# Optimization experiments

Measured on AMD Instinct MI355X. Metric: run time of the kernel, lower is better.

Reference implementation:

```python
import jax, jax.numpy as jnp
import numpy as np
from jax import lax

V = 128     # vocab_size
E = 512     # embed_size
H = 1024    # hidden_size
NE = 10     # num_experts
B = 32
S = 1024


def setup_inputs() -> dict:
    key = jax.random.key(0)
    ks = jax.random.split(key, 11)
    s = 0.05
    return {
        "x": jax.random.randint(ks[0], (B, S), 0, V),
        "emb": jax.random.normal(ks[1], (V, E), jnp.float32) * s,
        "W_ih": jax.random.normal(ks[2], (4 * H, E), jnp.float32) * s,   # gates i,f,g,o
        "W_hh": jax.random.normal(ks[3], (4 * H, H), jnp.float32) * s,
        "b_ih": jax.random.normal(ks[4], (4 * H,), jnp.float32) * s,
        "b_hh": jax.random.normal(ks[5], (4 * H,), jnp.float32) * s,
        "We": jax.random.normal(ks[6], (NE, V, H), jnp.float32) * s,    # expert Linear weights
        "be": jax.random.normal(ks[7], (NE, V), jnp.float32) * s,
        "Wg": jax.random.normal(ks[8], (NE, H), jnp.float32) * s,       # gating Linear
        "bg": jax.random.normal(ks[9], (NE,), jnp.float32) * s,
    }


def _lstm(xe, W_ih, W_hh, b_ih, b_hh):
    # xe: [B,S,E] -> hidden states [B,S,H]; PyTorch LSTM gate order i,f,g,o
    pre = jnp.einsum("bse,ge->bsg", xe, W_ih) + b_ih  # [B,S,4H], input proj hoisted out of scan
    h0 = jnp.zeros((xe.shape[0], H), xe.dtype)
    c0 = jnp.zeros((xe.shape[0], H), xe.dtype)

    def step(carry, p):
        h, c = carry
        g = p + h @ W_hh.T + b_hh
        i, f, gg, o = jnp.split(g, 4, axis=-1)
        c = jax.nn.sigmoid(f) * c + jax.nn.sigmoid(i) * jnp.tanh(gg)
        h = jax.nn.sigmoid(o) * jnp.tanh(c)
        return (h, c), h

    _, hs = lax.scan(step, (h0, c0), pre.transpose(1, 0, 2))  # scan over S
    return hs.transpose(1, 0, 2)  # [B,S,H]


def reference(x, emb, W_ih, W_hh, b_ih, b_hh, We, be, Wg, bg):
    xe = emb[x]                                   # [B,S,E]
    h = _lstm(xe, W_ih, W_hh, b_ih, b_hh)         # [B,S,H]
    # all experts as one batched GEMM: [NE,B,S,V]
    expert_outputs = jnp.einsum("bsh,evh->ebsv", h, We) + be[:, None, None, :]
    gating_weights = jax.nn.softmax(h[:, -1, :] @ Wg.T + bg, axis=-1)  # [B,NE]
    combined = jnp.einsum("be,ebsv->bsv", gating_weights, expert_outputs)
    return combined, expert_outputs, gating_weights
```

## Files before the change

kernel.cpp:

```cpp
#include <hip/hip_runtime.h>
#include <hip/hip_bf16.h>
#include <math.h>

#define V_  128
#define E_  512
#define H_  1024
#define NE_ 10
#define B_  32
#define S_  1024
#define G4H (4*H_)

typedef short bf16x8 __attribute__((ext_vector_type(8)));
typedef float f32x4  __attribute__((ext_vector_type(4)));
typedef int   i32x4  __attribute__((ext_vector_type(4)));

__device__ __forceinline__ short f2bf(float f) {
    __hip_bfloat16 h = __float2bfloat16(f);
    short s; __builtin_memcpy(&s, &h, 2); return s;
}
__device__ __forceinline__ float bf2f(ushort u) {
    unsigned int x = ((unsigned int)u) << 16;
    float f; __builtin_memcpy(&f, &x, 4); return f;
}
__device__ __forceinline__ float sigf(float x) { return 1.f / (1.f + __expf(-x)); }
__device__ __forceinline__ float tanhfast(float x) { return 1.f - 2.f / (__expf(2.f * x) + 1.f); }

__device__ __forceinline__ i32x4 gload4_sc(const void* p) {
    i32x4 r;
    asm volatile("global_load_dwordx4 %0, %1, off sc1" : "=&v"(r) : "v"(p));
    return r;
}
__device__ __forceinline__ void gstore4_sc(void* p, i32x4 v) {
    asm volatile("global_store_dwordx4 %0, %1, off sc1" :: "v"(p), "v"(v) : "memory");
}
__device__ __forceinline__ void gstore1_sc(void* p, int v) {
    asm volatile("global_store_dword %0, %1, off sc1" :: "v"(p), "v"(v) : "memory");
}
#define WAITCNT0() do { asm volatile("s_waitcnt vmcnt(0)" ::: "memory"); \
                        __builtin_amdgcn_sched_barrier(0); } while (0)

__global__ __launch_bounds__(256) void build_T(
    const float* __restrict__ emb, const float* __restrict__ W_ih,
    const float* __restrict__ b_ih, float* __restrict__ T2)
{
    int idx = blockIdx.x * 256 + threadIdx.x;
    int g = idx >> 7, v = idx & 127;
    const float* er = emb + v * E_;
    const float* wr = W_ih + (size_t)g * E_;
    float acc = b_ih[g];
    #pragma unroll 4
    for (int e = 0; e < E_; ++e) acc += er[e] * wr[e];
    T2[v * G4H + (g & 1023) * 4 + (g >> 10)] = acc;
}

__global__ __launch_bounds__(256) void conv_bf16(
    const float* __restrict__ src, ushort* __restrict__ dst, int n)
{
    int i = blockIdx.x * 256 + threadIdx.x;
    if (i < n) dst[i] = (ushort)f2bf(src[i]);
}

__global__ __launch_bounds__(512) void lstm_scan(
    const int* __restrict__ x, const float* __restrict__ T2,
    const float* __restrict__ W_hh, const float* __restrict__ b_hh,
    ushort* __restrict__ hbuf, ushort* __restrict__ h_all, int* __restrict__ flags)
{
    const int p = blockIdx.x;
    const int tid = threadIdx.x;
    const int lane = tid & 63, wave = tid >> 6;
    const int m = lane & 15, kg = lane >> 4;
    const int bh = wave & 1, kq = wave >> 1;

    __shared__ __align__(16) ushort Wl[32 * 1024];
    __shared__ float  part[8 * 512];
    __shared__ __align__(16) float pre_s[32][36];
    __shared__ __align__(16) ushort hstage[256];
    __shared__ float  bhh_l[32];

    #pragma unroll
    for (int i = 0; i < 8; ++i) {
        int grp = tid + i * 512;
        int r = grp >> 7, k8 = (grp & 127) * 8;
        const float* wsrc = W_hh + (size_t)((r & 3) * H_ + p * 8 + (r >> 2)) * H_ + k8;
        float4 w0 = *(const float4*)wsrc;
        float4 w1 = *(const float4*)(wsrc + 4);
        bf16x8 a;
        a[0]=f2bf(w0.x); a[1]=f2bf(w0.y); a[2]=f2bf(w0.z); a[3]=f2bf(w0.w);
        a[4]=f2bf(w1.x); a[5]=f2bf(w1.y); a[6]=f2bf(w1.z); a[7]=f2bf(w1.w);
        *(bf16x8*)&Wl[r * 1024 + (k8 ^ ((r & 7) << 3))] = a;
    }
    if (tid < 32) bhh_l[tid] = b_hh[(tid & 3) * H_ + p * 8 + (tid >> 2)];

    int boff[8];
    #pragma unroll
    for (int kk = 0; kk < 8; ++kk)
        boff[kk] = (bh * 16 + m) * 1024 + kq * 256 + kk * 32 + kg * 8;

    const int eb = tid >> 3, eu = tid & 7;
    float cst = 0.f;
    ushort* hb0 = hbuf;
    ushort* hb1 = hbuf + B_ * H_;
    const int swz = (m & 7) << 3;
    __syncthreads();

    for (int t = 0; t < S_; ++t) {
        const ushort* hrd = (t & 1) ? hb0 : hb1;
        ushort*       hwr = (t & 1) ? hb1 : hb0;

        {
            const int src = kq * 32 + (lane & 31);
            const int* fp = flags + src * 16;
            for (;;) {
                int f;
                asm volatile("global_load_dword %0, %1, off sc1\n\ts_waitcnt vmcnt(0)"
                             : "=&v"(f) : "v"(fp) : "memory");
                __builtin_amdgcn_sched_barrier(0);
                if (__all(f >= t)) break;
                __builtin_amdgcn_s_sleep(1);
            }
        }

        i32x4 braw[8];
        #pragma unroll
        for (int kk = 0; kk < 8; ++kk) braw[kk] = gload4_sc(hrd + boff[kk]);
        WAITCNT0();

        f32x4 acc0 = {0.f,0.f,0.f,0.f}, acc1 = {0.f,0.f,0.f,0.f};
        #pragma unroll
        for (int kk = 0; kk < 8; ++kk) {
            int koff = (kq * 256 + kk * 32 + kg * 8) ^ swz;
            bf16x8 a0 = *(const bf16x8*)&Wl[m * 1024 + koff];
            bf16x8 a1 = *(const bf16x8*)&Wl[(16 + m) * 1024 + koff];
            bf16x8 bv; __builtin_memcpy(&bv, &braw[kk], 16);
            acc0 = __builtin_amdgcn_mfma_f32_16x16x32_bf16(a0, bv, acc0, 0, 0, 0);
            acc1 = __builtin_amdgcn_mfma_f32_16x16x32_bf16(a1, bv, acc1, 0, 0, 0);
        }
        {
            float* pw = part + wave * 512;
            #pragma unroll
            for (int d = 0; d < 4; ++d) {
                pw[(kg * 4 + d) * 16 + m]       = acc0[d];
                pw[256 + (kg * 4 + d) * 16 + m] = acc1[d];
            }
        }
        __syncthreads();

        #pragma unroll
        for (int i = 0; i < 2; ++i) {
            int flat = tid + i * 512;
            float s = part[flat] + part[1024 + flat] + part[2048 + flat] + part[3072 + flat];
            int b = ((flat >> 9) & 1) * 16 + (flat & 15);
            int r = ((flat >> 8) & 1) * 16 + ((flat >> 4) & 15);
            pre_s[b][r] = s;
        }
        __syncthreads();

        if (tid < 256) {
            int xv = x[eb * S_ + t];
            float4 tv = *(const float4*)(T2 + (size_t)xv * G4H + (size_t)(p * 8 + eu) * 4);
            float4 pv = *(const float4*)&pre_s[eb][eu * 4];
            int r0 = eu * 4;
            float pi = pv.x + tv.x + bhh_l[r0 + 0];
            float pf = pv.y + tv.y + bhh_l[r0 + 1];
            float pg = pv.z + tv.z + bhh_l[r0 + 2];
            float po = pv.w + tv.w + bhh_l[r0 + 3];
            cst = sigf(pf) * cst + sigf(pi) * tanhfast(pg);
            float h = sigf(po) * tanhfast(cst);
            unsigned int hb16 = (unsigned int)(unsigned short)f2bf(h);
            unsigned int hn = (unsigned int)__shfl_xor((int)hb16, 1);
            if (!(eu & 1))
                *(unsigned int*)(h_all + (size_t)eb * (S_ * H_) + (size_t)t * H_ + (p * 8 + eu))
                    = hb16 | (hn << 16);
            hstage[tid] = (ushort)hb16;
        }
        __syncthreads();

        if (t == S_ - 1) break;

        if (wave == 0) {
            if (lane < 32) {
                i32x4 v = *(const i32x4*)&hstage[lane * 8];
                gstore4_sc(hwr + lane * 1024 + p * 8, v);
            }
            asm volatile("s_waitcnt vmcnt(0)" ::: "memory");
            if (lane == 0) gstore1_sc(flags + p * 16, t + 1);
        }
    }
}

__global__ __launch_bounds__(256) void expert_gemm(
    const ushort* __restrict__ A, const ushort* __restrict__ Bw,
    const float* __restrict__ be, float* __restrict__ out)
{
    __shared__ ushort As[128][40];
    __shared__ ushort Bs[128][40];
    const int tid = threadIdx.x;
    const int bm = blockIdx.x / 10, bn = blockIdx.x % 10;
    const int m0 = bm * 128, n0 = bn * 128;
    const int lane = tid & 63, wave = tid >> 6;
    const int wm = wave >> 1, wn = wave & 1;
    const int fm = lane & 15, kg = lane >> 4;

    const int srow = tid >> 1, scol = (tid & 1) * 16;
    const ushort* Ag = A  + (size_t)(m0 + srow) * H_ + scol;
    const ushort* Bg = Bw + (size_t)(n0 + srow) * H_ + scol;

    f32x4 acc[4][4];
    #pragma unroll
    for (int i = 0; i < 4; ++i)
        #pragma unroll
        for (int j = 0; j < 4; ++j) acc[i][j] = (f32x4){0.f,0.f,0.f,0.f};

    int4 ra0 = *(const int4*)(Ag),     ra1 = *(const int4*)(Ag + 8);
    int4 rb0 = *(const int4*)(Bg),     rb1 = *(const int4*)(Bg + 8);

    for (int k0 = 0; k0 < H_; k0 += 32) {
        __syncthreads();
        *(int4*)&As[srow][scol] = ra0;  *(int4*)&As[srow][scol + 8] = ra1;
        *(int4*)&Bs[srow][scol] = rb0;  *(int4*)&Bs[srow][scol + 8] = rb1;
        __syncthreads();
        if (k0 + 32 < H_) {
            ra0 = *(const int4*)(Ag + k0 + 32);  ra1 = *(const int4*)(Ag + k0 + 40);
            rb0 = *(const int4*)(Bg + k0 + 32);  rb1 = *(const int4*)(Bg + k0 + 40);
        }
        bf16x8 af[4], bfv[4];
        #pragma unroll
        for (int i = 0; i < 4; ++i) af[i] = *(const bf16x8*)&As[wm * 64 + i * 16 + fm][kg * 8];
        #pragma unroll
        for (int j = 0; j < 4; ++j) bfv[j] = *(const bf16x8*)&Bs[wn * 64 + j * 16 + fm][kg * 8];
        #pragma unroll
        for (int i = 0; i < 4; ++i)
            #pragma unroll
            for (int j = 0; j < 4; ++j)
                acc[i][j] = __builtin_amdgcn_mfma_f32_16x16x32_bf16(af[i], bfv[j], acc[i][j], 0, 0, 0);
    }

    const int e = bn;
    const size_t ebase = (size_t)e * ((size_t)B_ * S_ * V_);
    #pragma unroll
    for (int i = 0; i < 4; ++i) {
        #pragma unroll
        for (int d = 0; d < 4; ++d) {
            int row = m0 + wm * 64 + i * 16 + kg * 4 + d;
            float* orow = out + ebase + (size_t)row * V_;
            #pragma unroll
            for (int j = 0; j < 4; ++j) {
                int col = wn * 64 + j * 16 + fm;
                orow[col] = acc[i][j][d] + be[n0 + col];
            }
        }
    }
}

__global__ __launch_bounds__(256) void gating_kernel(
    const ushort* __restrict__ h_all, const float* __restrict__ Wg,
    const float* __restrict__ bg, float* __restrict__ gate_out)
{
    int b = blockIdx.x;
    int tid = threadIdx.x;
    __shared__ float red[NE_][256];
    const ushort* h = h_all + (size_t)b * (S_ * H_) + (size_t)(S_ - 1) * H_;
    float pa[NE_];
    #pragma unroll
    for (int e = 0; e < NE_; ++e) pa[e] = 0.f;
    for (int k = tid; k < H_; k += 256) {
        float hv = bf2f(h[k]);
        #pragma unroll
        for (int e = 0; e < NE_; ++e) pa[e] += hv * Wg[e * H_ + k];
    }
    #pragma unroll
    for (int e = 0; e < NE_; ++e) red[e][tid] = pa[e];
    __syncthreads();
    for (int s = 128; s > 0; s >>= 1) {
        if (tid < s) {
            #pragma unroll
            for (int e = 0; e < NE_; ++e) red[e][tid] += red[e][tid + s];
        }
        __syncthreads();
    }
    if (tid == 0) {
        float lg[NE_], mx = -1e30f;
        #pragma unroll
        for (int e = 0; e < NE_; ++e) { lg[e] = red[e][0] + bg[e]; mx = fmaxf(mx, lg[e]); }
        float s = 0.f;
        #pragma unroll
        for (int e = 0; e < NE_; ++e) { lg[e] = expf(lg[e] - mx); s += lg[e]; }
        #pragma unroll
        for (int e = 0; e < NE_; ++e) gate_out[b * NE_ + e] = lg[e] / s;
    }
}

__global__ __launch_bounds__(256) void combine_kernel(
    const float* __restrict__ exp_out, const float* __restrict__ gate,
    float* __restrict__ comb)
{
    int idx = blockIdx.x * 256 + threadIdx.x;
    int b = idx >> 17;
    float acc = 0.f;
    #pragma unroll
    for (int e = 0; e < NE_; ++e)
        acc += gate[b * NE_ + e] * exp_out[(size_t)e * (size_t)(B_ * S_ * V_) + idx];
    comb[idx] = acc;
}

extern "C" void kernel_launch(void* const* d_in, const int* in_sizes, int n_in,
                              void* d_out, int out_size, void* d_ws, size_t ws_size,
                              hipStream_t stream)
{
    const int*   x    = (const int*)  d_in[0];
    const float* emb  = (const float*)d_in[1];
    const float* W_ih = (const float*)d_in[2];
    const float* W_hh = (const float*)d_in[3];
    const float* b_ih = (const float*)d_in[4];
    const float* b_hh = (const float*)d_in[5];
    const float* We   = (const float*)d_in[6];
    const float* be   = (const float*)d_in[7];
    const float* Wg   = (const float*)d_in[8];
    const float* bg   = (const float*)d_in[9];

    float* out     = (float*)d_out;
    float* comb    = out;
    float* exp_out = out + 4194304;
    float* gate    = out + 4194304 + 41943040;

    char*   ws    = (char*)d_ws;
    float*  T2    = (float*)ws;
    ushort* hbuf  = (ushort*)(ws + (2u << 20));
    int*    flags = (int*)   (ws + (2u << 20) + (128u << 10));
    ushort* We_bf = (ushort*)(ws + (4u << 20));
    ushort* h_all = (ushort*)(ws + (8u << 20));

    (void)hipMemsetAsync(ws + (2u << 20), 0, (136u << 10), stream);

    build_T      <<<2048, 256, 0, stream>>>(emb, W_ih, b_ih, T2);
    conv_bf16    <<<(NE_ * V_ * H_ + 255) / 256, 256, 0, stream>>>(We, We_bf, NE_ * V_ * H_);
    lstm_scan    <<<128, 512, 0, stream>>>(x, T2, W_hh, b_hh, hbuf, h_all, flags);
    expert_gemm  <<<256 * 10, 256, 0, stream>>>(h_all, We_bf, be, exp_out);
    gating_kernel<<<B_, 256, 0, stream>>>(h_all, Wg, bg, gate);
    combine_kernel<<<4194304 / 256, 256, 0, stream>>>(exp_out, gate, comb);
}
```

Baseline: 4.985 ms.

## Reorder W_hh LDS layout, pad partials, share flag polling, prefetch input gates

Stores the W_hh slice in LDS in MFMA-fragment order so each lane reads contiguous 16-byte chunks instead of XOR-swizzled rows. Pads the partial-sum buffer to stride 17 to avoid bank conflicts in the cross-wave reduction. Only half the waves now poll the global flags, then signal the others through a workgroup-scope LDS atomic, which cuts global polling traffic. The token and input-gate table loads are issued before the MFMA loop so their latency overlaps the recurrent matmul. The extra intra-block spin wait adds latency and a deadlock risk if the waves fall out of step.

After: 5.208 ms. +4.5%, slower.

```diff
diff --git a/kernel.cpp b/kernel.cpp
--- a/kernel.cpp
+++ b/kernel.cpp
@@ -71,25 +71,31 @@
     const int m = lane & 15, kg = lane >> 4;
     const int bh = wave & 1, kq = wave >> 1;
 
-    __shared__ __align__(16) ushort Wl[32 * 1024];
-    __shared__ float  part[8 * 512];
-    __shared__ __align__(16) float pre_s[32][36];
+    __shared__ __align__(16) ushort Wl[32768];
+    __shared__ float  part[8 * 544];
+    __shared__ __align__(16) float preF[1024];
     __shared__ __align__(16) ushort hstage[256];
     __shared__ float  bhh_l[32];
+    __shared__ int    eps4[4];
 
     #pragma unroll
     for (int i = 0; i < 8; ++i) {
         int grp = tid + i * 512;
-        int r = grp >> 7, k8 = (grp & 127) * 8;
+        int r = grp >> 7, kglob = grp & 127;
+        int k8 = kglob * 8;
         const float* wsrc = W_hh + (size_t)((r & 3) * H_ + p * 8 + (r >> 2)) * H_ + k8;
         float4 w0 = *(const float4*)wsrc;
         float4 w1 = *(const float4*)(wsrc + 4);
         bf16x8 a;
         a[0]=f2bf(w0.x); a[1]=f2bf(w0.y); a[2]=f2bf(w0.z); a[3]=f2bf(w0.w);
         a[4]=f2bf(w1.x); a[5]=f2bf(w1.y); a[6]=f2bf(w1.z); a[7]=f2bf(w1.w);
-        *(bf16x8*)&Wl[r * 1024 + (k8 ^ ((r & 7) << 3))] = a;
+        int tile = r >> 4, mm = r & 15;
+        int kq2 = kglob >> 5, kk = (kglob >> 2) & 7, kg2 = kglob & 3;
+        int frag = ((tile * 4 + kq2) * 8 + kk) * 4 + kg2;
+        *(bf16x8*)&Wl[(frag * 16 + mm) * 8] = a;
     }
     if (tid < 32) bhh_l[tid] = b_hh[(tid & 3) * H_ + p * 8 + (tid >> 2)];
+    if (tid < 4)  eps4[tid] = 0;
 
     int boff[8];
     #pragma unroll
@@ -100,14 +106,13 @@
     float cst = 0.f;
     ushort* hb0 = hbuf;
     ushort* hb1 = hbuf + B_ * H_;
-    const int swz = (m & 7) << 3;
     __syncthreads();
 
     for (int t = 0; t < S_; ++t) {
         const ushort* hrd = (t & 1) ? hb0 : hb1;
         ushort*       hwr = (t & 1) ? hb1 : hb0;
 
-        {
+        if (bh == 0) {
             const int src = kq * 32 + (lane & 31);
             const int* fp = flags + src * 16;
             for (;;) {
@@ -118,6 +123,16 @@
                 if (__all(f >= t)) break;
                 __builtin_amdgcn_s_sleep(1);
             }
+            __hip_atomic_store(&eps4[kq], t, __ATOMIC_RELEASE, __HIP_MEMORY_SCOPE_WORKGROUP);
+        } else {
+            while (__hip_atomic_load(&eps4[kq], __ATOMIC_ACQUIRE, __HIP_MEMORY_SCOPE_WORKGROUP) < t)
+                __builtin_amdgcn_s_sleep(1);
+        }
+
+        int xv = 0; float4 tv = {0.f, 0.f, 0.f, 0.f};
+        if (tid < 256) {
+            xv = x[eb * S_ + t];
+            tv = *(const float4*)(T2 + (size_t)xv * G4H + (size_t)(p * 8 + eu) * 4);
         }
 
         i32x4 braw[8];
@@ -128,19 +143,20 @@
         f32x4 acc0 = {0.f,0.f,0.f,0.f}, acc1 = {0.f,0.f,0.f,0.f};
         #pragma unroll
         for (int kk = 0; kk < 8; ++kk) {
-            int koff = (kq * 256 + kk * 32 + kg * 8) ^ swz;
-            bf16x8 a0 = *(const bf16x8*)&Wl[m * 1024 + koff];
-            bf16x8 a1 = *(const bf16x8*)&Wl[(16 + m) * 1024 + koff];
+            int f0 = ((0 * 4 + kq) * 8 + kk) * 4 + kg;
+            int f1 = ((1 * 4 + kq) * 8 + kk) * 4 + kg;
+            bf16x8 a0 = *(const bf16x8*)&Wl[(f0 * 16 + m) * 8];
+            bf16x8 a1 = *(const bf16x8*)&Wl[(f1 * 16 + m) * 8];
             bf16x8 bv; __builtin_memcpy(&bv, &braw[kk], 16);
             acc0 = __builtin_amdgcn_mfma_f32_16x16x32_bf16(a0, bv, acc0, 0, 0, 0);
             acc1 = __builtin_amdgcn_mfma_f32_16x16x32_bf16(a1, bv, acc1, 0, 0, 0);
         }
         {
-            float* pw = part + wave * 512;
+            float* pw = part + wave * 544;
             #pragma unroll
             for (int d = 0; d < 4; ++d) {
-                pw[(kg * 4 + d) * 16 + m]       = acc0[d];
-                pw[256 + (kg * 4 + d) * 16 + m] = acc1[d];
+                pw[(kg * 4 + d) * 17 + m]       = acc0[d];
+                pw[272 + (kg * 4 + d) * 17 + m] = acc1[d];
             }
         }
         __syncthreads();
@@ -148,17 +164,17 @@
         #pragma unroll
         for (int i = 0; i < 2; ++i) {
             int flat = tid + i * 512;
-            float s = part[flat] + part[1024 + flat] + part[2048 + flat] + part[3072 + flat];
-            int b = ((flat >> 9) & 1) * 16 + (flat & 15);
-            int r = ((flat >> 8) & 1) * 16 + ((flat >> 4) & 15);
-            pre_s[b][r] = s;
+            int b = flat & 31, r = flat >> 5;
+            int bh2 = b >> 4, mm = b & 15, tile = r >> 4, row16 = r & 15;
+            int off = tile * 272 + row16 * 17 + mm;
+            float s = part[(0 * 2 + bh2) * 544 + off] + part[(1 * 2 + bh2) * 544 + off]
+                    + part[(2 * 2 + bh2) * 544 + off] + part[(3 * 2 + bh2) * 544 + off];
+            preF[b * 32 + r] = s;
         }
         __syncthreads();
 
         if (tid < 256) {
-            int xv = x[eb * S_ + t];
-            float4 tv = *(const float4*)(T2 + (size_t)xv * G4H + (size_t)(p * 8 + eu) * 4);
-            float4 pv = *(const float4*)&pre_s[eb][eu * 4];
+            float4 pv = *(const float4*)&preF[tid * 4];
             int r0 = eu * 4;
             float pi = pv.x + tv.x + bhh_l[r0 + 0];
             float pf = pv.y + tv.y + bhh_l[r0 + 1];
```

## Replace per-step flag polling with tagged hidden-state words in LSTM scan

Applied to the files above, without the earlier changes.

Removes the separate flag array and the flag-spin-then-load sequence in the persistent LSTM scan. Each bf16 hidden value is now stored in a 32-bit word whose upper half carries the timestep tag, so consumers poll the data itself and retry only chunks whose tags are stale. This drops one round trip and the producer's store-wait-flag sequence per step. In exchange it doubles the exchange buffer size and adds tag checking and repacking before the MFMAs. The T2 embedding lookup is also hoisted before the matmul to overlap its latency.

Measured after the change: 9.924 ms. 99.1% more time.

```diff
diff --git a/kernel.cpp b/kernel.cpp
--- a/kernel.cpp
+++ b/kernel.cpp
@@ -32,9 +32,6 @@
 }
 __device__ __forceinline__ void gstore4_sc(void* p, i32x4 v) {
     asm volatile("global_store_dwordx4 %0, %1, off sc1" :: "v"(p), "v"(v) : "memory");
-}
-__device__ __forceinline__ void gstore1_sc(void* p, int v) {
-    asm volatile("global_store_dword %0, %1, off sc1" :: "v"(p), "v"(v) : "memory");
 }
 #define WAITCNT0() do { asm volatile("s_waitcnt vmcnt(0)" ::: "memory"); \
                         __builtin_amdgcn_sched_barrier(0); } while (0)
@@ -63,7 +60,7 @@
 __global__ __launch_bounds__(512) void lstm_scan(
     const int* __restrict__ x, const float* __restrict__ T2,
     const float* __restrict__ W_hh, const float* __restrict__ b_hh,
-    ushort* __restrict__ hbuf, ushort* __restrict__ h_all, int* __restrict__ flags)
+    unsigned int* __restrict__ tagbuf, ushort* __restrict__ h_all)
 {
     const int p = blockIdx.x;
     const int tid = threadIdx.x;
@@ -91,47 +88,66 @@
     }
     if (tid < 32) bhh_l[tid] = b_hh[(tid & 3) * H_ + p * 8 + (tid >> 2)];
 
-    int boff[8];
-    #pragma unroll
-    for (int kk = 0; kk < 8; ++kk)
-        boff[kk] = (bh * 16 + m) * 1024 + kq * 256 + kk * 32 + kg * 8;
+    int off16[16];
+    #pragma unroll
+    for (int kk = 0; kk < 8; ++kk) {
+        int base = (bh * 16 + m) * 1024 + kq * 256 + kk * 32 + kg * 8;
+        off16[kk * 2]     = base;
+        off16[kk * 2 + 1] = base + 4;
+    }
 
     const int eb = tid >> 3, eu = tid & 7;
     float cst = 0.f;
-    ushort* hb0 = hbuf;
-    ushort* hb1 = hbuf + B_ * H_;
+    unsigned int* tb0 = tagbuf;
+    unsigned int* tb1 = tagbuf + 32 * 1024;
     const int swz = (m & 7) << 3;
     __syncthreads();
 
     for (int t = 0; t < S_; ++t) {
-        const ushort* hrd = (t & 1) ? hb0 : hb1;
-        ushort*       hwr = (t & 1) ? hb1 : hb0;
-
-        {
-            const int src = kq * 32 + (lane & 31);
-            const int* fp = flags + src * 16;
-            for (;;) {
-                int f;
-                asm volatile("global_load_dword %0, %1, off sc1\n\ts_waitcnt vmcnt(0)"
-                             : "=&v"(f) : "v"(fp) : "memory");
-                __builtin_amdgcn_sched_barrier(0);
-                if (__all(f >= t)) break;
-                __builtin_amdgcn_s_sleep(1);
-            }
-        }
-
-        i32x4 braw[8];
-        #pragma unroll
-        for (int kk = 0; kk < 8; ++kk) braw[kk] = gload4_sc(hrd + boff[kk]);
-        WAITCNT0();
+        const unsigned int* trd = (t & 1) ? tb0 : tb1;
+        unsigned int*       twr = (t & 1) ? tb1 : tb0;
+
+        i32x4 braw[16];
+        const unsigned int exp_tag = (unsigned int)t;
+        unsigned int pend = 0xFFFFu;
+        for (;;) {
+            #pragma unroll
+            for (int i = 0; i < 16; ++i)
+                if (pend & (1u << i))
+                    braw[i] = gload4_sc(trd + off16[i]);
+            WAITCNT0();
+            #pragma unroll
+            for (int i = 0; i < 16; ++i)
+                if (pend & (1u << i)) {
+                    unsigned int bad = (((unsigned int)braw[i][0]) >> 16) ^ exp_tag;
+                    bad |= (((unsigned int)braw[i][1]) >> 16) ^ exp_tag;
+                    bad |= (((unsigned int)braw[i][2]) >> 16) ^ exp_tag;
+                    bad |= (((unsigned int)braw[i][3]) >> 16) ^ exp_tag;
+                    if (bad == 0) pend &= ~(1u << i);
+                }
+            if (__all(pend == 0)) break;
+            __builtin_amdgcn_s_sleep(1);
+        }
+
+        int xv = 0; float4 tv = {0.f, 0.f, 0.f, 0.f};
+        if (tid < 256) {
+            xv = x[eb * S_ + t];
+            tv = *(const float4*)(T2 + (size_t)xv * G4H + (size_t)(p * 8 + eu) * 4);
+        }
 
         f32x4 acc0 = {0.f,0.f,0.f,0.f}, acc1 = {0.f,0.f,0.f,0.f};
         #pragma unroll
         for (int kk = 0; kk < 8; ++kk) {
+            i32x4 lo = braw[kk * 2], hi = braw[kk * 2 + 1];
+            i32x4 fv;
+            fv[0] = (lo[0] & 0xFFFF) | (lo[1] << 16);
+            fv[1] = (lo[2] & 0xFFFF) | (lo[3] << 16);
+            fv[2] = (hi[0] & 0xFFFF) | (hi[1] << 16);
+            fv[3] = (hi[2] & 0xFFFF) | (hi[3] << 16);
+            bf16x8 bv; __builtin_memcpy(&bv, &fv, 16);
             int koff = (kq * 256 + kk * 32 + kg * 8) ^ swz;
             bf16x8 a0 = *(const bf16x8*)&Wl[m * 1024 + koff];
             bf16x8 a1 = *(const bf16x8*)&Wl[(16 + m) * 1024 + koff];
-            bf16x8 bv; __builtin_memcpy(&bv, &braw[kk], 16);
             acc0 = __builtin_amdgcn_mfma_f32_16x16x32_bf16(a0, bv, acc0, 0, 0, 0);
             acc1 = __builtin_amdgcn_mfma_f32_16x16x32_bf16(a1, bv, acc1, 0, 0, 0);
         }
@@ -156,8 +172,6 @@
         __syncthreads();
 
         if (tid < 256) {
-            int xv = x[eb * S_ + t];
-            float4 tv = *(const float4*)(T2 + (size_t)xv * G4H + (size_t)(p * 8 + eu) * 4);
             float4 pv = *(const float4*)&pre_s[eb][eu * 4];
             int r0 = eu * 4;
             float pi = pv.x + tv.x + bhh_l[r0 + 0];
@@ -177,13 +191,17 @@
 
         if (t == S_ - 1) break;
 
-        if (wave == 0) {
-            if (lane < 32) {
-                i32x4 v = *(const i32x4*)&hstage[lane * 8];
-                gstore4_sc(hwr + lane * 1024 + p * 8, v);
-            }
-            asm volatile("s_waitcnt vmcnt(0)" ::: "memory");
-            if (lane == 0) gstore1_sc(flags + p * 16, t + 1);
+        if (wave == 0 && lane < 32) {
+            const ushort* hs8 = &hstage[lane * 8];
+            unsigned int tg = ((unsigned int)(t + 1)) << 16;
+            i32x4 v0, v1;
+            v0[0] = (int)(hs8[0] | tg); v0[1] = (int)(hs8[1] | tg);
+            v0[2] = (int)(hs8[2] | tg); v0[3] = (int)(hs8[3] | tg);
+            v1[0] = (int)(hs8[4] | tg); v1[1] = (int)(hs8[5] | tg);
+            v1[2] = (int)(hs8[6] | tg); v1[3] = (int)(hs8[7] | tg);
+            unsigned int* dst = twr + lane * 1024 + p * 8;
+            gstore4_sc(dst, v0);
+            gstore4_sc(dst + 4, v1);
         }
     }
 }
@@ -323,18 +341,17 @@
     float* exp_out = out + 4194304;
     float* gate    = out + 4194304 + 41943040;
 
-    char*   ws    = (char*)d_ws;
-    float*  T2    = (float*)ws;
-    ushort* hbuf  = (ushort*)(ws + (2u << 20));
-    int*    flags = (int*)   (ws + (2u << 20) + (128u << 10));
-    ushort* We_bf = (ushort*)(ws + (4u << 20));
-    ushort* h_all = (ushort*)(ws + (8u << 20));
-
-    (void)hipMemsetAsync(ws + (2u << 20), 0, (136u << 10), stream);
+    char*         ws     = (char*)d_ws;
+    float*        T2     = (float*)ws;
+    unsigned int* tagbuf = (unsigned int*)(ws + (2u << 20));
+    ushort*       We_bf  = (ushort*)(ws + (4u << 20));
+    ushort*       h_all  = (ushort*)(ws + (8u << 20));
+
+    (void)hipMemsetAsync(ws + (2u << 20), 0, (256u << 10), stream);
 
     build_T      <<<2048, 256, 0, stream>>>(emb, W_ih, b_ih, T2);
     conv_bf16    <<<(NE_ * V_ * H_ + 255) / 256, 256, 0, stream>>>(We, We_bf, NE_ * V_ * H_);
-    lstm_scan    <<<128, 512, 0, stream>>>(x, T2, W_hh, b_hh, hbuf, h_all, flags);
+    lstm_scan    <<<128, 512, 0, stream>>>(x, T2, W_hh, b_hh, tagbuf, h_all);
     expert_gemm  <<<256 * 10, 256, 0, stream>>>(h_all, We_bf, be, exp_out);
     gating_kernel<<<B_, 256, 0, stream>>>(h_all, Wg, bg, gate);
     combine_kernel<<<4194304 / 256, 256, 0, stream>>>(exp_out, gate, comb);
```
